# Kernel tuning notes

Measured on AMD Instinct MI355X. Metric: run time of the kernel, lower is better.

Reference implementation:

```python
import jax, jax.numpy as jnp
import numpy as np

HEADS = 8
HDIM = 64
MAX_PEMB = 512


def setup_inputs() -> dict:
    key = jax.random.key(0)
    ks = jax.random.split(key, 6)
    B, S, D = 4, 1024, 512
    return {
        "x": jax.random.normal(ks[0], (B, S, D), jnp.float32),
        "attn_mask": jnp.ones((B, S), jnp.bool_),
        "Wq": jax.random.normal(ks[1], (D, HEADS * HDIM), jnp.float32) * 0.02,
        "Wkv": jax.random.normal(ks[2], (D, 2 * HEADS * HDIM), jnp.float32) * 0.02,
        "Wout": jax.random.normal(ks[3], (HEADS * HDIM, D), jnp.float32) * 0.02,
        "bout": jnp.zeros((D,), jnp.float32),
        "pemb": jax.random.normal(ks[4], (2 * MAX_PEMB + 1, HDIM), jnp.float32) * 0.02,
    }


def reference(x, attn_mask, Wq, Wkv, Wout, bout, pemb):
    # attn_mask is unpacked but unused in the original call(); faithful to source.
    B, S, D = x.shape
    scale = HDIM ** (-0.5)

    q = (x @ Wq).reshape(B, S, HEADS, HDIM).transpose(0, 2, 1, 3)  # [B,H,S,hd]
    kv = x @ Wkv
    k, v = jnp.split(kv, 2, axis=-1)
    k = k.reshape(B, S, HEADS, HDIM).transpose(0, 2, 1, 3)
    v = v.reshape(B, S, HEADS, HDIM).transpose(0, 2, 1, 3)

    attn_score = jnp.einsum('bhqd,bhkd->bhqk', q, k) * scale

    seq = jnp.arange(S)
    dist = jnp.clip(seq[:, None] - seq[None, :], -MAX_PEMB, MAX_PEMB) + MAX_PEMB  # [S,S]
    rel_pemb = pemb[dist]  # [S,S,hd]
    pos_attn = jnp.einsum('bhsd,std->bhst', q, rel_pemb) * scale  # [B,H,S,S]

    attn_probs = jax.nn.softmax(attn_score + pos_attn, axis=-1)
    ctx = jnp.einsum('bhqk,bhkd->bqhd', attn_probs, v).reshape(B, S, HEADS * HDIM)
    return ctx @ Wout + bout
```

## Files before the change

kernel.cpp:

```cpp
#include <hip/hip_runtime.h>
#include <hip/hip_bf16.h>

constexpr int BATCH = 4;
constexpr int SEQ   = 1024;
constexpr int DM    = 512;
constexpr int NH    = 8;
constexpr int HD    = 64;
constexpr int NQKV  = 1536;

typedef unsigned short u16;
typedef __attribute__((ext_vector_type(8))) __bf16 bf8;
typedef __attribute__((ext_vector_type(4))) __bf16 bf4;
typedef __attribute__((ext_vector_type(4))) float  f4;
typedef __attribute__((ext_vector_type(16))) float f16v;

#define MFMA16(a, b, c) __builtin_amdgcn_mfma_f32_16x16x32_bf16(a, b, c, 0, 0, 0)
#define MFMA32(a, b, c) __builtin_amdgcn_mfma_f32_32x32x16_bf16(a, b, c, 0, 0, 0)

#define QSC 0.18033688f

static __device__ __forceinline__ u16 f2b(float f) {
    union { float f; unsigned u; } v; v.f = f;
    unsigned r = v.u + 0x7FFFu + ((v.u >> 16) & 1u);
    return (u16)(r >> 16);
}
static __device__ __forceinline__ float b2f(u16 x) {
    union { unsigned u; float f; } v; v.u = (unsigned)x << 16;
    return v.f;
}
static __device__ __forceinline__ float fexp2(float x) {
    return __builtin_amdgcn_exp2f(x);
}
static __device__ __forceinline__ void gl_lds16(const void* g, void* l) {
    __builtin_amdgcn_global_load_lds(
        (const __attribute__((address_space(1))) void*)g,
        (__attribute__((address_space(3))) void*)l, 16, 0, 0);
}
static __device__ __forceinline__ unsigned cvtpk_bf16(float lo, float hi) {
    unsigned r;
    asm("v_cvt_pk_bf16_f32 %0, %1, %2" : "=v"(r) : "v"(lo), "v"(hi));
    return r;
}
static __device__ __forceinline__ void swap32(unsigned &a, unsigned &b) {
    asm("v_permlane32_swap_b32 %0, %1" : "+v"(a), "+v"(b));
}

__device__ __forceinline__ void tcvt_tile(const float* __restrict__ in,
                                          u16* __restrict__ out,
                                          int R, int C, int bx, int by, int tid,
                                          float (*t)[33]) {
    int r0 = by * 32, c0 = bx * 32;
    int lc = tid & 31, lr = tid >> 5;
    #pragma unroll
    for (int p = 0; p < 4; p++) {
        int r = lr + p * 8;
        t[r][lc] = in[(size_t)(r0 + r) * C + c0 + lc];
    }
    __syncthreads();
    #pragma unroll
    for (int p = 0; p < 4; p++) {
        int r = lr + p * 8;
        out[(size_t)(c0 + r) * R + r0 + lc] = f2b(t[lc][r]);
    }
}

__global__ __launch_bounds__(256)
void prep(const float* __restrict__ x, const float* __restrict__ Wq,
          const float* __restrict__ Wkv, const float* __restrict__ Wout,
          const float* __restrict__ pemb,
          u16* __restrict__ xb, u16* __restrict__ qkvw,
          u16* __restrict__ Woutt, u16* __restrict__ pembb) {
    __shared__ float t[32][33];
    const int blk = blockIdx.x, tid = threadIdx.x;
    if (blk < 2048) {
        int i = (blk * 256 + tid) * 4;
        float4 v = *(const float4*)(x + i);
        ushort4 o = {f2b(v.x), f2b(v.y), f2b(v.z), f2b(v.w)};
        *(ushort4*)(xb + i) = o;
    } else if (blk < 2113) {
        int i = ((blk - 2048) * 256 + tid) * 4;
        if (i < 1025 * HD) {
            float4 v = *(const float4*)(pemb + i);
            ushort4 o = {f2b(v.x), f2b(v.y), f2b(v.z), f2b(v.w)};
            *(ushort4*)(pembb + i) = o;
        }
    } else if (blk < 2369) {
        int l = blk - 2113;
        tcvt_tile(Wq, qkvw, 512, 512, l & 15, l >> 4, tid, t);
    } else if (blk < 2881) {
        int l = blk - 2369;
        tcvt_tile(Wkv, qkvw + 512 * 512, 512, 1024, l & 31, l >> 5, tid, t);
    } else {
        int l = blk - 2881;
        tcvt_tile(Wout, Woutt, 512, 512, l & 15, l >> 4, tid, t);
    }
}

template<int BN>
__global__ __launch_bounds__(256)
void gemm_bt(const u16* __restrict__ A, const u16* __restrict__ Bt,
             int M, int N, int K,
             float* __restrict__ Cf, const float* __restrict__ bias,
             __bf16* __restrict__ qtb, __bf16* __restrict__ ktb,
             __bf16* __restrict__ vtb) {
    constexpr int NJ = BN / 32;
    __shared__ __align__(16) u16 As[2][64][32];
    __shared__ __align__(16) u16 Bs[2][BN][32];
    const int tid = threadIdx.x, w = tid >> 6, lane = tid & 63;
    const int l15 = lane & 15, l4 = lane >> 4;
    const int wr = (w >> 1) * 32, wc = (w & 1) * (BN / 2);
    const int bm = blockIdx.y * 64, bn = blockIdx.x * BN;

    f4 acc[2][NJ];
    #pragma unroll
    for (int i = 0; i < 2; i++)
        #pragma unroll
        for (int j = 0; j < NJ; j++) acc[i][j] = (f4){0.f, 0.f, 0.f, 0.f};

    const int rS = lane >> 2;
    const int cS = (lane & 3) * 8;

    for (int k0 = 0; k0 < K; k0 += 64) {
        #pragma unroll
        for (int ks = 0; ks < 2; ks++) {
            gl_lds16(A + (size_t)(bm + w * 16 + rS) * K + k0 + ks * 32 + cS,
                     &As[ks][w * 16][0]);
            #pragma unroll
            for (int rb = 0; rb < BN / 4; rb += 16)
                gl_lds16(Bt + (size_t)(bn + w * (BN / 4) + rb + rS) * K
                             + k0 + ks * 32 + cS,
                         &Bs[ks][w * (BN / 4) + rb][0]);
        }
        __syncthreads();
        #pragma unroll
        for (int ks = 0; ks < 2; ks++) {
            bf8 af[2], bf[NJ];
            #pragma unroll
            for (int i = 0; i < 2; i++)
                af[i] = *(const bf8*)&As[ks][wr + i * 16 + l15][l4 * 8];
            #pragma unroll
            for (int j = 0; j < NJ; j++)
                bf[j] = *(const bf8*)&Bs[ks][wc + j * 16 + l15][l4 * 8];
            #pragma unroll
            for (int i = 0; i < 2; i++)
                #pragma unroll
                for (int j = 0; j < NJ; j++)
                    acc[i][j] = MFMA16(af[i], bf[j], acc[i][j]);
        }
        __syncthreads();
    }
    #pragma unroll
    for (int i = 0; i < 2; i++)
        #pragma unroll
        for (int j = 0; j < NJ; j++) {
            const int col = bn + wc + j * 16 + l15;
            const int row0 = bm + wr + i * 16 + l4 * 4;
            if (Cf) {
                #pragma unroll
                for (int reg = 0; reg < 4; reg++)
                    Cf[(size_t)(row0 + reg) * N + col] = acc[i][j][reg] + bias[col];
            } else if (col < 512) {
                int h = col >> 6, d = col & 63;
                #pragma unroll
                for (int reg = 0; reg < 4; reg++) {
                    int row = row0 + reg;
                    int b = row >> 10, t = row & 1023;
                    qtb[((((size_t)(b * 8 + h)) << 10 | t) << 6) | d] =
                        (__bf16)(acc[i][j][reg] * QSC);
                }
            } else if (col < 1024) {
                int h = (col >> 6) - 8, d = col & 63;
                #pragma unroll
                for (int reg = 0; reg < 4; reg++) {
                    int row = row0 + reg;
                    int b = row >> 10, t = row & 1023;
                    ktb[((((size_t)(b * 8 + h)) << 10 | t) << 6) | d] =
                        (__bf16)acc[i][j][reg];
                }
            } else {
                int h = (col >> 6) - 16, d = col & 63;
                int b = row0 >> 10, t = row0 & 1023;
                __bf16 pk[4];
                #pragma unroll
                for (int reg = 0; reg < 4; reg++) pk[reg] = (__bf16)acc[i][j][reg];
                *(ushort4*)&vtb[(((size_t)(b * 8 + h) * 64 + d) << 10) | t] =
                    *(ushort4*)pk;
            }
        }
}

__global__ __launch_bounds__(256)
void attn_mfma(const u16* __restrict__ qtb, const u16* __restrict__ ktb,
               const u16* __restrict__ vtb, const u16* __restrict__ pembb,
               __bf16* __restrict__ ctxb) {
    __shared__ __align__(16) __bf16 Kb[2][64][72];
    __shared__ __align__(16) __bf16 Vb[2][64][72];
    __shared__ __align__(16) __bf16 Qd[256][72];

    const int tid = threadIdx.x, w = tid >> 6, lane = tid & 63;
    const int l31 = lane & 31, hi = lane >> 5;
    const int wq = w >> 1, wt = w & 1;
    const int bh = blockIdx.x, b = bh >> 3;
    const int s0 = blockIdx.y * 64;

    bf8 qb[4];
    {
        const u16* qp = qtb + ((size_t)bh * SEQ + s0 + wq * 32 + l31) * HD + hi * 8;
        #pragma unroll
        for (int st = 0; st < 4; st++) qb[st] = *(const bf8*)(qp + st * 16);
    }

    #pragma unroll
    for (int pass = 0; pass < 2; pass++) {
        const int jr = s0 + 449 + pass * 64 + wt * 32 + l31;
        const int jc = min(1024, max(0, jr));
        const u16* pp = pembb + (size_t)jc * HD + hi * 8;
        f16v acc;
        #pragma unroll
        for (int r = 0; r < 16; r++) acc[r] = 0.f;
        #pragma unroll
        for (int st = 0; st < 4; st++) {
            bf8 pj = *(const bf8*)(pp + st * 16);
            acc = MFMA32(qb[st], pj, acc);
        }
        #pragma unroll
        for (int o4 = 0; o4 < 4; o4++) {
            bf4 pk;
            #pragma unroll
            for (int r = 0; r < 4; r++) pk[r] = (__bf16)acc[o4 * 4 + r];
            *(bf4*)&Qd[jr & 255][wq * 32 + o4 * 8 + hi * 4] = pk;
        }
    }

    float l_lane = 0.f;
    f16v oo[2];
    #pragma unroll
    for (int dt = 0; dt < 2; dt++)
        #pragma unroll
        for (int r = 0; r < 16; r++) oo[dt][r] = 0.f;

    const u16* kbase = ktb + (size_t)bh * SEQ * HD;
    const u16* vbase = vtb + (size_t)bh * HD * SEQ;
    const int sr = tid >> 3, sc = (tid & 7) * 8;

    *(bf8*)&Kb[0][sr][sc]      = *(const bf8*)(kbase + (size_t)sr * HD + sc);
    *(bf8*)&Kb[0][sr + 32][sc] = *(const bf8*)(kbase + (size_t)(sr + 32) * HD + sc);
    *(bf8*)&Vb[0][sr][sc]      = *(const bf8*)(vbase + (size_t)sr * SEQ + sc);
    *(bf8*)&Vb[0][sr + 32][sc] = *(const bf8*)(vbase + (size_t)(sr + 32) * SEQ + sc);
    __syncthreads();

    for (int i = 0; i < 16; i++) {
        const int cur = i & 1, nxt = cur ^ 1;
        const int t0 = i * 64, t1 = t0 + 64;
        const bool pre = (i < 15);
        bf8 kr0, kr1, vr0, vr1, pj0, pj1, pj2, pj3;
        const int jrn = s0 + 449 - 64 * (i + 1) + wt * 32 + l31;
        if (pre) {
            kr0 = *(const bf8*)(kbase + (size_t)(t1 + sr) * HD + sc);
            kr1 = *(const bf8*)(kbase + (size_t)(t1 + sr + 32) * HD + sc);
            vr0 = *(const bf8*)(vbase + (size_t)sr * SEQ + t1 + sc);
            vr1 = *(const bf8*)(vbase + (size_t)(sr + 32) * SEQ + t1 + sc);
            const int jc = min(1024, max(0, jrn));
            const u16* pp = pembb + (size_t)jc * HD + hi * 8;
            pj0 = *(const bf8*)(pp);
            pj1 = *(const bf8*)(pp + 16);
            pj2 = *(const bf8*)(pp + 32);
            pj3 = *(const bf8*)(pp + 48);
        }

        bf8 ka[4];
        #pragma unroll
        for (int st = 0; st < 4; st++)
            ka[st] = *(const bf8*)&Kb[cur][wt * 32 + l31][st * 16 + hi * 8];
        const int jcst = (s0 - t0 + 512) + wq * 32 + l31 - wt * 32 - 4 * hi;
        const u16* qdc = (const u16*)&Qd[0][0] + wq * 32 + l31;
        u16 rg[16];
        #pragma unroll
        for (int r = 0; r < 16; r++) {
            const int pat = (r & 3) + 8 * (r >> 2);
            rg[r] = qdc[((jcst - pat) & 255) * 72];
        }
        bf8 vf00 = *(const bf8*)&Vb[cur][l31][wt * 32 + hi * 8];
        bf8 vf01 = *(const bf8*)&Vb[cur][l31][wt * 32 + 16 + hi * 8];
        bf8 vf10 = *(const bf8*)&Vb[cur][32 + l31][wt * 32 + hi * 8];
        bf8 vf11 = *(const bf8*)&Vb[cur][32 + l31][wt * 32 + 16 + hi * 8];

        __builtin_amdgcn_s_setprio(1);
        f16v s16;
        #pragma unroll
        for (int r = 0; r < 16; r++) s16[r] = 0.f;
        #pragma unroll
        for (int st = 0; st < 4; st++) s16 = MFMA32(ka[st], qb[st], s16);

        float p[16];
        float la = 0.f, lb = 0.f;
        #pragma unroll
        for (int r = 0; r < 8; r++) {
            float pv = fexp2(s16[r] + b2f(rg[r]));
            p[r] = pv; la += pv;
        }
        unsigned w00 = cvtpk_bf16(p[0], p[1]), w01 = cvtpk_bf16(p[2], p[3]);
        unsigned w10 = cvtpk_bf16(p[4], p[5]), w11 = cvtpk_bf16(p[6], p[7]);
        swap32(w00, w10); swap32(w01, w11);
        union { unsigned u[4]; bf8 v; } pa0, pa1;
        pa0.u[0] = w00; pa0.u[1] = w01; pa0.u[2] = w10; pa0.u[3] = w11;
        oo[0] = MFMA32(pa0.v, vf00, oo[0]);
        oo[1] = MFMA32(pa0.v, vf10, oo[1]);
        #pragma unroll
        for (int r = 8; r < 16; r++) {
            float pv = fexp2(s16[r] + b2f(rg[r]));
            p[r] = pv; lb += pv;
        }
        unsigned w20 = cvtpk_bf16(p[8],  p[9]),  w21 = cvtpk_bf16(p[10], p[11]);
        unsigned w30 = cvtpk_bf16(p[12], p[13]), w31 = cvtpk_bf16(p[14], p[15]);
        swap32(w20, w30); swap32(w21, w31);
        pa1.u[0] = w20; pa1.u[1] = w21; pa1.u[2] = w30; pa1.u[3] = w31;
        oo[0] = MFMA32(pa1.v, vf01, oo[0]);
        oo[1] = MFMA32(pa1.v, vf11, oo[1]);
        __builtin_amdgcn_s_setprio(0);
        l_lane += la + lb;

        if (pre) {
            f16v rf;
            #pragma unroll
            for (int r = 0; r < 16; r++) rf[r] = 0.f;
            rf = MFMA32(qb[0], pj0, rf);
            rf = MFMA32(qb[1], pj1, rf);
            rf = MFMA32(qb[2], pj2, rf);
            rf = MFMA32(qb[3], pj3, rf);
            #pragma unroll
            for (int o4 = 0; o4 < 4; o4++) {
                bf4 pk;
                #pragma unroll
                for (int r = 0; r < 4; r++) pk[r] = (__bf16)rf[o4 * 4 + r];
                *(bf4*)&Qd[jrn & 255][wq * 32 + o4 * 8 + hi * 4] = pk;
            }
            *(bf8*)&Kb[nxt][sr][sc]      = kr0;
            *(bf8*)&Kb[nxt][sr + 32][sc] = kr1;
            *(bf8*)&Vb[nxt][sr][sc]      = vr0;
            *(bf8*)&Vb[nxt][sr + 32][sc] = vr1;
        }
        __syncthreads();
    }

    float lsum = l_lane + __shfl_xor(l_lane, 32);
    float* Os = (float*)&Qd[0][0];
    float* Ls = Os + 4096;
    if (lane < 32) Ls[(wq * 2 + wt) * 32 + l31] = lsum;
    if (wt == 0) {
        #pragma unroll
        for (int dt = 0; dt < 2; dt++)
            #pragma unroll
            for (int r = 0; r < 16; r++) {
                const int q = (r & 3) + 8 * (r >> 2) + 4 * hi;
                Os[(wq * 32 + q) * 64 + dt * 32 + l31] = oo[dt][r];
            }
    }
    __syncthreads();
    if (wt == 1) {
        const int h = bh & 7;
        #pragma unroll
        for (int r = 0; r < 16; r++) {
            const int q = (r & 3) + 8 * (r >> 2) + 4 * hi;
            const float li = 1.f / (Ls[wq * 64 + q] + Ls[wq * 64 + 32 + q]);
            #pragma unroll
            for (int dt = 0; dt < 2; dt++) {
                float v = (oo[dt][r] + Os[(wq * 32 + q) * 64 + dt * 32 + l31]) * li;
                ctxb[(size_t)(b * SEQ + s0 + wq * 32 + q) * DM + h * HD + dt * 32 + l31]
                    = (__bf16)v;
            }
        }
    }
}

extern "C" void kernel_launch(void* const* d_in, const int* in_sizes, int n_in,
                              void* d_out, int out_size, void* d_ws, size_t ws_size,
                              hipStream_t stream) {
    const float* x    = (const float*)d_in[0];
    const float* Wq   = (const float*)d_in[2];
    const float* Wkv  = (const float*)d_in[3];
    const float* Wout = (const float*)d_in[4];
    const float* bout = (const float*)d_in[5];
    const float* pemb = (const float*)d_in[6];
    float* out = (float*)d_out;

    const int M = BATCH * SEQ;
    u16* p = (u16*)d_ws;
    u16* xb    = p; p += (size_t)M * DM;
    u16* qkvw  = p; p += (size_t)NQKV * DM;
    u16* Woutt = p; p += (size_t)DM * DM;
    u16* pembb = p; p += (size_t)1025 * HD;
    u16* qtb   = p; p += (size_t)M * DM;
    u16* ktb   = p; p += (size_t)M * DM;
    u16* vtb   = p; p += (size_t)M * DM;
    u16* ctxb  = p; p += (size_t)M * DM;

    prep<<<3137, 256, 0, stream>>>(x, Wq, Wkv, Wout, pemb, xb, qkvw, Woutt, pembb);

    gemm_bt<128><<<dim3(NQKV / 128, M / 64), 256, 0, stream>>>(
        xb, qkvw, M, NQKV, DM, nullptr, nullptr,
        (__bf16*)qtb, (__bf16*)ktb, (__bf16*)vtb);

    attn_mfma<<<dim3(BATCH * NH, SEQ / 64), 256, 0, stream>>>(
        qtb, ktb, vtb, pembb, (__bf16*)ctxb);

    gemm_bt<64><<<dim3(DM / 64, M / 64), 256, 0, stream>>>(
        ctxb, Woutt, M, DM, DM, out, bout, nullptr, nullptr, nullptr);
}
```

Baseline: 124.6 us.

## Load K/V tiles directly global-to-LDS with XOR-swizzled unpadded layout

Replaces the register-staged K/V prefetch (global load into VGPRs, then LDS store after compute) with direct global-to-LDS loads through the gl_lds16 helper. The padded 72-wide LDS rows become unpadded 64-wide rows, and an XOR swizzle on the 8-element chunk index avoids bank conflicts. The MFMA operand reads are updated to match the swizzle. The intent is to cut VGPR pressure and the explicit LDS store instructions. The risk is that the async LDS writes must complete before the barrier, which depends on how the helper waits.

```diff
diff --git a/kernel.cpp b/kernel.cpp
--- a/kernel.cpp
+++ b/kernel.cpp
@@ -193,8 +193,8 @@
 void attn_mfma(const u16* __restrict__ qtb, const u16* __restrict__ ktb,
                const u16* __restrict__ vtb, const u16* __restrict__ pembb,
                __bf16* __restrict__ ctxb) {
-    __shared__ __align__(16) __bf16 Kb[2][64][72];
-    __shared__ __align__(16) __bf16 Vb[2][64][72];
+    __shared__ __align__(16) __bf16 Kb[2][64][64];
+    __shared__ __align__(16) __bf16 Vb[2][64][64];
     __shared__ __align__(16) __bf16 Qd[256][72];
 
     const int tid = threadIdx.x, w = tid >> 6, lane = tid & 63;
@@ -202,6 +202,10 @@
     const int wq = w >> 1, wt = w & 1;
     const int bh = blockIdx.x, b = bh >> 3;
     const int s0 = blockIdx.y * 64;
+    const int m7 = l31 & 7;
+
+    const int srow = lane >> 3;
+    const int sswz = ((lane & 7) ^ srow) * 8;
 
     bf8 qb[4];
     {
@@ -241,25 +245,30 @@
 
     const u16* kbase = ktb + (size_t)bh * SEQ * HD;
     const u16* vbase = vtb + (size_t)bh * HD * SEQ;
-    const int sr = tid >> 3, sc = (tid & 7) * 8;
-
-    *(bf8*)&Kb[0][sr][sc]      = *(const bf8*)(kbase + (size_t)sr * HD + sc);
-    *(bf8*)&Kb[0][sr + 32][sc] = *(const bf8*)(kbase + (size_t)(sr + 32) * HD + sc);
-    *(bf8*)&Vb[0][sr][sc]      = *(const bf8*)(vbase + (size_t)sr * SEQ + sc);
-    *(bf8*)&Vb[0][sr + 32][sc] = *(const bf8*)(vbase + (size_t)(sr + 32) * SEQ + sc);
+
+    #pragma unroll
+    for (int G = 0; G < 2; G++) {
+        const int r0 = w * 16 + G * 8;
+        gl_lds16(kbase + (size_t)(r0 + srow) * HD + sswz, &Kb[0][r0][0]);
+        gl_lds16(vbase + (size_t)(r0 + srow) * SEQ + sswz, &Vb[0][r0][0]);
+    }
     __syncthreads();
 
     for (int i = 0; i < 16; i++) {
         const int cur = i & 1, nxt = cur ^ 1;
         const int t0 = i * 64, t1 = t0 + 64;
         const bool pre = (i < 15);
-        bf8 kr0, kr1, vr0, vr1, pj0, pj1, pj2, pj3;
+        bf8 pj0, pj1, pj2, pj3;
         const int jrn = s0 + 449 - 64 * (i + 1) + wt * 32 + l31;
         if (pre) {
-            kr0 = *(const bf8*)(kbase + (size_t)(t1 + sr) * HD + sc);
-            kr1 = *(const bf8*)(kbase + (size_t)(t1 + sr + 32) * HD + sc);
-            vr0 = *(const bf8*)(vbase + (size_t)sr * SEQ + t1 + sc);
-            vr1 = *(const bf8*)(vbase + (size_t)(sr + 32) * SEQ + t1 + sc);
+            #pragma unroll
+            for (int G = 0; G < 2; G++) {
+                const int r0 = w * 16 + G * 8;
+                gl_lds16(kbase + (size_t)(t1 + r0 + srow) * HD + sswz,
+                         &Kb[nxt][r0][0]);
+                gl_lds16(vbase + (size_t)(r0 + srow) * SEQ + t1 + sswz,
+                         &Vb[nxt][r0][0]);
+            }
             const int jc = min(1024, max(0, jrn));
             const u16* pp = pembb + (size_t)jc * HD + hi * 8;
             pj0 = *(const bf8*)(pp);
@@ -271,7 +280,7 @@
         bf8 ka[4];
         #pragma unroll
         for (int st = 0; st < 4; st++)
-            ka[st] = *(const bf8*)&Kb[cur][wt * 32 + l31][st * 16 + hi * 8];
+            ka[st] = *(const bf8*)&Kb[cur][wt * 32 + l31][((st * 2 + hi) ^ m7) * 8];
         const int jcst = (s0 - t0 + 512) + wq * 32 + l31 - wt * 32 - 4 * hi;
         const u16* qdc = (const u16*)&Qd[0][0] + wq * 32 + l31;
         u16 rg[16];
@@ -280,10 +289,10 @@
             const int pat = (r & 3) + 8 * (r >> 2);
             rg[r] = qdc[((jcst - pat) & 255) * 72];
         }
-        bf8 vf00 = *(const bf8*)&Vb[cur][l31][wt * 32 + hi * 8];
-        bf8 vf01 = *(const bf8*)&Vb[cur][l31][wt * 32 + 16 + hi * 8];
-        bf8 vf10 = *(const bf8*)&Vb[cur][32 + l31][wt * 32 + hi * 8];
-        bf8 vf11 = *(const bf8*)&Vb[cur][32 + l31][wt * 32 + 16 + hi * 8];
+        bf8 vf00 = *(const bf8*)&Vb[cur][l31][((wt * 4 + hi) ^ m7) * 8];
+        bf8 vf01 = *(const bf8*)&Vb[cur][l31][((wt * 4 + 2 + hi) ^ m7) * 8];
+        bf8 vf10 = *(const bf8*)&Vb[cur][32 + l31][((wt * 4 + hi) ^ m7) * 8];
+        bf8 vf11 = *(const bf8*)&Vb[cur][32 + l31][((wt * 4 + 2 + hi) ^ m7) * 8];
 
         __builtin_amdgcn_s_setprio(1);
         f16v s16;
@@ -335,10 +344,6 @@
                 for (int r = 0; r < 4; r++) pk[r] = (__bf16)rf[o4 * 4 + r];
                 *(bf4*)&Qd[jrn & 255][wq * 32 + o4 * 8 + hi * 4] = pk;
             }
-            *(bf8*)&Kb[nxt][sr][sc]      = kr0;
-            *(bf8*)&Kb[nxt][sr + 32][sc] = kr1;
-            *(bf8*)&Vb[nxt][sr][sc]      = vr0;
-            *(bf8*)&Vb[nxt][sr + 32][sc] = vr1;
         }
         __syncthreads();
     }
```

After: 128.5 us. +3.1%, slower.
